# Kernel optimization log

Hardware: AMD Instinct MI355X
Metric: run time of the kernel (lower is better)

The kernel has to match this reference:

```python
import jax, jax.numpy as jnp
import numpy as np

MASK_SIZE = 28
IMG_H, IMG_W = 520, 704
NUM_GT = 128
NUM_PROP = 512


def box_iou(a, b):
    # a: [P,4], b: [G,4] in xyxy -> [P,G]
    area_a = (a[:, 2] - a[:, 0]) * (a[:, 3] - a[:, 1])
    area_b = (b[:, 2] - b[:, 0]) * (b[:, 3] - b[:, 1])
    lt = jnp.maximum(a[:, None, :2], b[None, :, :2])
    rb = jnp.minimum(a[:, None, 2:], b[None, :, 2:])
    wh = jnp.clip(rb - lt, 0.0)
    inter = wh[..., 0] * wh[..., 1]
    return inter / (area_a[:, None] + area_b[None, :] - inter)


def crop_resize_one(box, gidx, gt_masks):
    # Faithful to extract_mask_target: int-truncate box, clamp, crop, bilinear
    # resize (align_corners=False) to MASK_SIZE x MASK_SIZE.
    S = MASK_SIZE
    H, W = gt_masks.shape[1], gt_masks.shape[2]
    x1 = jnp.clip(box[0].astype(jnp.int32), 0, W - 1)
    y1 = jnp.clip(box[1].astype(jnp.int32), 0, H - 1)
    x2 = jnp.maximum(x1 + 1, jnp.minimum(box[2].astype(jnp.int32), W))
    y2 = jnp.maximum(y1 + 1, jnp.minimum(box[3].astype(jnp.int32), H))
    cwi = x2 - x1
    chi = y2 - y1
    cw = cwi.astype(jnp.float32)
    ch = chi.astype(jnp.float32)
    j = jnp.arange(S, dtype=jnp.float32)
    # source coords inside crop, border-clamped (PyTorch bilinear, align_corners=False)
    sx = jnp.clip((j + 0.5) * cw / S - 0.5, 0.0, cw - 1.0)
    sy = jnp.clip((j + 0.5) * ch / S - 0.5, 0.0, ch - 1.0)
    x0 = jnp.floor(sx)
    y0 = jnp.floor(sy)
    wx = sx - x0
    wy = sy - y0
    x0i = x0.astype(jnp.int32)
    y0i = y0.astype(jnp.int32)
    x1i = jnp.minimum(x0i + 1, cwi - 1)
    y1i = jnp.minimum(y0i + 1, chi - 1)
    m = gt_masks[gidx]  # [H, W]
    ax0 = x0i + x1
    ax1 = x1i + x1
    ay0 = y0i + y1
    ay1 = y1i + y1
    v00 = m[ay0[:, None], ax0[None, :]]
    v01 = m[ay0[:, None], ax1[None, :]]
    v10 = m[ay1[:, None], ax0[None, :]]
    v11 = m[ay1[:, None], ax1[None, :]]
    top = (1.0 - wx)[None, :] * v00 + wx[None, :] * v01
    bot = (1.0 - wx)[None, :] * v10 + wx[None, :] * v11
    return (1.0 - wy)[:, None] * top + wy[:, None] * bot  # [S, S]


def setup_inputs() -> dict:
    key = jax.random.key(0)
    k1, k2, k3, k4, k5 = jax.random.split(key, 5)
    # GT boxes: cell-like boxes inside a 520x704 image
    cx = jax.random.uniform(k1, (NUM_GT,), minval=50.0, maxval=IMG_W - 50.0)
    cy = jax.random.uniform(k2, (NUM_GT,), minval=50.0, maxval=IMG_H - 50.0)
    wh = jax.random.uniform(k3, (NUM_GT, 2), minval=20.0, maxval=80.0)
    gt_boxes = jnp.stack([cx - wh[:, 0] / 2, cy - wh[:, 1] / 2,
                          cx + wh[:, 0] / 2, cy + wh[:, 1] / 2], axis=1)
    # proposals: jittered copies of GT boxes -> realistic positive fraction
    reps = NUM_PROP // NUM_GT
    noise = jax.random.normal(k4, (NUM_PROP, 4)) * 4.0
    proposals = jnp.tile(gt_boxes, (reps, 1)) + noise
    # per-instance binary masks (float, as .float() in the torch code)
    gt_masks = (jax.random.uniform(k5, (NUM_GT, IMG_H, IMG_W)) < 0.3).astype(jnp.float32)
    mask_logits = jax.random.normal(jax.random.fold_in(key, 7),
                                    (NUM_PROP, 2, MASK_SIZE, MASK_SIZE), dtype=jnp.float32)
    return {"proposals": proposals, "gt_boxes": gt_boxes,
            "gt_masks": gt_masks, "mask_logits": mask_logits}


def reference(proposals, gt_boxes, gt_masks, mask_logits):
    S = MASK_SIZE
    ious = box_iou(proposals, gt_boxes)           # [P, G]
    max_ious = ious.max(axis=1)
    matched = jnp.argmax(ious, axis=1)            # [P]
    pos = (max_ious > 0.5).astype(jnp.float32)    # [P]
    matched_boxes = gt_boxes[matched]             # [P, 4]
    # batched crop + bilinear resize of matched GT masks (RoI-style gather)
    targets = jax.vmap(crop_resize_one, in_axes=(0, 0, None))(matched_boxes, matched, gt_masks)  # [P,S,S]
    logits = mask_logits[:, 1]                    # foreground channel [P,S,S]
    # stable BCE with logits
    bce = jnp.maximum(logits, 0.0) - logits * targets + jnp.log1p(jnp.exp(-jnp.abs(logits)))
    npos = pos.sum()
    loss_pos = jnp.sum(bce * pos[:, None, None]) / (jnp.maximum(npos, 1.0) * S * S)
    loss_neg = jnp.mean(mask_logits ** 2) * 0.01
    return jnp.where(npos > 0, loss_pos, loss_neg)
```

## Files before the change

kernel.cpp:

```cpp
#include <hip/hip_runtime.h>
#include <math.h>

#define NUM_GT   128
#define NUM_PROP 512
#define IMG_H    520
#define IMG_W    704
#define MS       28
#define LOGITS_N (NUM_PROP * 2 * MS * MS)

#define WS_MATCHED_OFF 256
#define WS_POS_OFF     (256 + NUM_PROP * 4)
#define WS_ZERO_BYTES  (256 + NUM_PROP * 8)

__global__ void match_kernel(const float* __restrict__ proposals,
                             const float* __restrict__ gt_boxes,
                             int* __restrict__ matched,
                             float* __restrict__ pos,
                             float* __restrict__ npos) {
    __shared__ float gb[NUM_GT * 4];
    for (int i = threadIdx.x; i < NUM_GT * 4; i += blockDim.x) gb[i] = gt_boxes[i];
    __syncthreads();

    int p = blockIdx.x * blockDim.x + threadIdx.x;
    if (p >= NUM_PROP) return;

    float ax1 = proposals[p * 4 + 0];
    float ay1 = proposals[p * 4 + 1];
    float ax2 = proposals[p * 4 + 2];
    float ay2 = proposals[p * 4 + 3];
    float area_a = (ax2 - ax1) * (ay2 - ay1);

    float best = -1e30f;
    int bi = 0;
    for (int g = 0; g < NUM_GT; ++g) {
        float bx1 = gb[g * 4 + 0];
        float by1 = gb[g * 4 + 1];
        float bx2 = gb[g * 4 + 2];
        float by2 = gb[g * 4 + 3];
        float area_b = (bx2 - bx1) * (by2 - by1);
        float ltx = fmaxf(ax1, bx1), lty = fmaxf(ay1, by1);
        float rbx = fminf(ax2, bx2), rby = fminf(ay2, by2);
        float w = fmaxf(rbx - ltx, 0.0f);
        float h = fmaxf(rby - lty, 0.0f);
        float inter = w * h;
        float iou = inter / (area_a + area_b - inter);
        if (iou > best) { best = iou; bi = g; }
    }
    matched[p] = bi;
    float ps = (best > 0.5f) ? 1.0f : 0.0f;
    pos[p] = ps;
    atomicAdd(npos, ps);
}

__global__ void bce_kernel(const float* __restrict__ gt_boxes,
                           const float* __restrict__ gt_masks,
                           const float* __restrict__ mask_logits,
                           const int* __restrict__ matched,
                           const float* __restrict__ pos,
                           float* __restrict__ bce_sum) {
    const int p = blockIdx.x;
    const int t = threadIdx.x;

    __shared__ int   s_gidx;
    __shared__ int   s_x0[MS], s_x1[MS], s_y0[MS], s_y1[MS];
    __shared__ float s_wx[MS], s_wy[MS];
    __shared__ float red[4];

    if (t == 0) s_gidx = matched[p];
    __syncthreads();
    const int g = s_gidx;

    const float b0 = gt_boxes[g * 4 + 0];
    const float b1 = gt_boxes[g * 4 + 1];
    const float b2 = gt_boxes[g * 4 + 2];
    const float b3 = gt_boxes[g * 4 + 3];

    int x1 = min(max((int)b0, 0), IMG_W - 1);
    int y1 = min(max((int)b1, 0), IMG_H - 1);
    int x2 = max(x1 + 1, min((int)b2, IMG_W));
    int y2 = max(y1 + 1, min((int)b3, IMG_H));
    int cwi = x2 - x1;
    int chi = y2 - y1;
    float cw = (float)cwi;
    float ch = (float)chi;

    if (t < MS) {
        float j = (float)t + 0.5f;
        float sx = fminf(fmaxf(j * cw / 28.0f - 0.5f, 0.0f), cw - 1.0f);
        float x0f = floorf(sx);
        int x0i = (int)x0f;
        s_wx[t] = sx - x0f;
        s_x0[t] = x0i + x1;
        s_x1[t] = min(x0i + 1, cwi - 1) + x1;

        float sy = fminf(fmaxf(j * ch / 28.0f - 0.5f, 0.0f), ch - 1.0f);
        float y0f = floorf(sy);
        int y0i = (int)y0f;
        s_wy[t] = sy - y0f;
        s_y0[t] = y0i + y1;
        s_y1[t] = min(y0i + 1, chi - 1) + y1;
    }
    __syncthreads();

    const float* m  = gt_masks + (size_t)g * IMG_H * IMG_W;
    const float* lg = mask_logits + ((size_t)p * 2 + 1) * (MS * MS);

    float acc = 0.0f;
    for (int idx = t; idx < MS * MS; idx += blockDim.x) {
        int i = idx / MS;
        int j = idx - i * MS;
        float wx = s_wx[j], wy = s_wy[i];
        const float* r0 = m + (size_t)s_y0[i] * IMG_W;
        const float* r1 = m + (size_t)s_y1[i] * IMG_W;
        int cx0 = s_x0[j], cx1 = s_x1[j];
        float v00 = r0[cx0], v01 = r0[cx1];
        float v10 = r1[cx0], v11 = r1[cx1];
        float top = (1.0f - wx) * v00 + wx * v01;
        float bot = (1.0f - wx) * v10 + wx * v11;
        float tv  = (1.0f - wy) * top + wy * bot;
        float l = lg[idx];
        float bce = fmaxf(l, 0.0f) - l * tv + log1pf(expf(-fabsf(l)));
        acc += bce;
    }

    float v = acc;
    #pragma unroll
    for (int o = 32; o > 0; o >>= 1) v += __shfl_down(v, o, 64);
    int lane = t & 63, wid = t >> 6;
    if (lane == 0) red[wid] = v;
    __syncthreads();
    if (t == 0) {
        float s = red[0] + red[1] + red[2] + red[3];
        atomicAdd(bce_sum, s * pos[p]);
    }
}

__global__ void sq_kernel(const float* __restrict__ mask_logits,
                          float* __restrict__ sqsum) {
    const int nvec = LOGITS_N / 4;
    const float4* src = (const float4*)mask_logits;
    float acc = 0.0f;
    for (int i = blockIdx.x * blockDim.x + threadIdx.x; i < nvec;
         i += gridDim.x * blockDim.x) {
        float4 x = src[i];
        acc += x.x * x.x + x.y * x.y + x.z * x.z + x.w * x.w;
    }
    float v = acc;
    #pragma unroll
    for (int o = 32; o > 0; o >>= 1) v += __shfl_down(v, o, 64);
    __shared__ float red[4];
    int lane = threadIdx.x & 63, wid = threadIdx.x >> 6;
    if (lane == 0) red[wid] = v;
    __syncthreads();
    if (threadIdx.x == 0) {
        float s = red[0] + red[1] + red[2] + red[3];
        atomicAdd(sqsum, s);
    }
}

__global__ void final_kernel(const float* __restrict__ acc, float* __restrict__ out) {
    float bce  = acc[0];
    float npos = acc[1];
    float sq   = acc[2];
    float loss_pos = bce / (fmaxf(npos, 1.0f) * (float)(MS * MS));
    float loss_neg = (sq / (float)LOGITS_N) * 0.01f;
    out[0] = (npos > 0.0f) ? loss_pos : loss_neg;
}

extern "C" void kernel_launch(void* const* d_in, const int* in_sizes, int n_in,
                              void* d_out, int out_size, void* d_ws, size_t ws_size,
                              hipStream_t stream) {
    const float* proposals   = (const float*)d_in[0];
    const float* gt_boxes    = (const float*)d_in[1];
    const float* gt_masks    = (const float*)d_in[2];
    const float* mask_logits = (const float*)d_in[3];
    float* out = (float*)d_out;

    float* acc     = (float*)d_ws;
    int*   matched = (int*)((char*)d_ws + WS_MATCHED_OFF);
    float* pos     = (float*)((char*)d_ws + WS_POS_OFF);

    hipMemsetAsync(d_ws, 0, WS_ZERO_BYTES, stream);

    match_kernel<<<(NUM_PROP + 255) / 256, 256, 0, stream>>>(proposals, gt_boxes,
                                                             matched, pos, acc + 1);
    bce_kernel<<<NUM_PROP, 256, 0, stream>>>(gt_boxes, gt_masks, mask_logits,
                                             matched, pos, acc + 0);
    sq_kernel<<<128, 256, 0, stream>>>(mask_logits, acc + 2);
    final_kernel<<<1, 1, 0, stream>>>(acc, out);
}
```

Measured before the change: 249.5 us.

## Fuse matching, BCE, square-sum and finalize into one kernel

Merges the IoU matching, crop-resize BCE, squared-logit sum and final loss computation into a single per-proposal kernel. Each block computes IoUs for its proposal in parallel across GT boxes with a shared-memory argmax reduction, and uses a last-block-done counter to write the final output. This removes three extra kernel launches, the intermediate matched/pos buffers and the serialized 128-iteration loop per thread. The cost is redundant loading of GT boxes in every block and an extra fence-and-atomic completion scheme.

```diff
diff --git a/kernel.cpp b/kernel.cpp
--- a/kernel.cpp
+++ b/kernel.cpp
@@ -8,83 +8,86 @@
 #define MS       28
 #define LOGITS_N (NUM_PROP * 2 * MS * MS)
 
-#define WS_MATCHED_OFF 256
-#define WS_POS_OFF     (256 + NUM_PROP * 4)
-#define WS_ZERO_BYTES  (256 + NUM_PROP * 8)
 
-__global__ void match_kernel(const float* __restrict__ proposals,
-                             const float* __restrict__ gt_boxes,
-                             int* __restrict__ matched,
-                             float* __restrict__ pos,
-                             float* __restrict__ npos) {
-    __shared__ float gb[NUM_GT * 4];
-    for (int i = threadIdx.x; i < NUM_GT * 4; i += blockDim.x) gb[i] = gt_boxes[i];
-    __syncthreads();
-
-    int p = blockIdx.x * blockDim.x + threadIdx.x;
-    if (p >= NUM_PROP) return;
-
-    float ax1 = proposals[p * 4 + 0];
-    float ay1 = proposals[p * 4 + 1];
-    float ax2 = proposals[p * 4 + 2];
-    float ay2 = proposals[p * 4 + 3];
-    float area_a = (ax2 - ax1) * (ay2 - ay1);
-
-    float best = -1e30f;
-    int bi = 0;
-    for (int g = 0; g < NUM_GT; ++g) {
-        float bx1 = gb[g * 4 + 0];
-        float by1 = gb[g * 4 + 1];
-        float bx2 = gb[g * 4 + 2];
-        float by2 = gb[g * 4 + 3];
-        float area_b = (bx2 - bx1) * (by2 - by1);
-        float ltx = fmaxf(ax1, bx1), lty = fmaxf(ay1, by1);
-        float rbx = fminf(ax2, bx2), rby = fminf(ay2, by2);
-        float w = fmaxf(rbx - ltx, 0.0f);
-        float h = fmaxf(rby - lty, 0.0f);
-        float inter = w * h;
-        float iou = inter / (area_a + area_b - inter);
-        if (iou > best) { best = iou; bi = g; }
-    }
-    matched[p] = bi;
-    float ps = (best > 0.5f) ? 1.0f : 0.0f;
-    pos[p] = ps;
-    atomicAdd(npos, ps);
-}
-
-__global__ void bce_kernel(const float* __restrict__ gt_boxes,
-                           const float* __restrict__ gt_masks,
-                           const float* __restrict__ mask_logits,
-                           const int* __restrict__ matched,
-                           const float* __restrict__ pos,
-                           float* __restrict__ bce_sum) {
+__global__ __launch_bounds__(256)
+void fused_kernel(const float* __restrict__ proposals,
+                  const float* __restrict__ gt_boxes,
+                  const float* __restrict__ gt_masks,
+                  const float* __restrict__ mask_logits,
+                  float* __restrict__ acc,
+                  float* __restrict__ out) {
     const int p = blockIdx.x;
     const int t = threadIdx.x;
 
-    __shared__ int   s_gidx;
+    __shared__ float s_gb[NUM_GT * 4];
+    __shared__ float s_iou[NUM_GT];
+    __shared__ int   s_idx[NUM_GT];
+    __shared__ int   s_g;
+    __shared__ float s_pos;
     __shared__ int   s_x0[MS], s_x1[MS], s_y0[MS], s_y1[MS];
     __shared__ float s_wx[MS], s_wy[MS];
-    __shared__ float red[4];
+    __shared__ float red_bce[4], red_sq[4];
 
-    if (t == 0) s_gidx = matched[p];
+    for (int i = t; i < NUM_GT * 4; i += 256) s_gb[i] = gt_boxes[i];
+
+    const float4* lp = (const float4*)(mask_logits + (size_t)p * 2 * MS * MS);
+    float sqacc = 0.0f;
+    for (int i = t; i < (2 * MS * MS) / 4; i += 256) {
+        float4 x = lp[i];
+        sqacc += x.x * x.x + x.y * x.y + x.z * x.z + x.w * x.w;
+    }
+
     __syncthreads();
-    const int g = s_gidx;
 
-    const float b0 = gt_boxes[g * 4 + 0];
-    const float b1 = gt_boxes[g * 4 + 1];
-    const float b2 = gt_boxes[g * 4 + 2];
-    const float b3 = gt_boxes[g * 4 + 3];
+    const float ax1 = proposals[p * 4 + 0];
+    const float ay1 = proposals[p * 4 + 1];
+    const float ax2 = proposals[p * 4 + 2];
+    const float ay2 = proposals[p * 4 + 3];
+    if (t < NUM_GT) {
+        float area_a = (ax2 - ax1) * (ay2 - ay1);
+        float bx1 = s_gb[t * 4 + 0];
+        float by1 = s_gb[t * 4 + 1];
+        float bx2 = s_gb[t * 4 + 2];
+        float by2 = s_gb[t * 4 + 3];
+        float area_b = (bx2 - bx1) * (by2 - by1);
+        float w = fmaxf(fminf(ax2, bx2) - fmaxf(ax1, bx1), 0.0f);
+        float h = fmaxf(fminf(ay2, by2) - fmaxf(ay1, by1), 0.0f);
+        float inter = w * h;
+        s_iou[t] = inter / (area_a + area_b - inter);
+        s_idx[t] = t;
+    }
+    __syncthreads();
 
-    int x1 = min(max((int)b0, 0), IMG_W - 1);
-    int y1 = min(max((int)b1, 0), IMG_H - 1);
-    int x2 = max(x1 + 1, min((int)b2, IMG_W));
-    int y2 = max(y1 + 1, min((int)b3, IMG_H));
-    int cwi = x2 - x1;
-    int chi = y2 - y1;
-    float cw = (float)cwi;
-    float ch = (float)chi;
+    for (int s = NUM_GT / 2; s > 0; s >>= 1) {
+        if (t < s) {
+            float a = s_iou[t], b = s_iou[t + s];
+            int ia = s_idx[t], ib = s_idx[t + s];
+            if (b > a || (b == a && ib < ia)) { s_iou[t] = b; s_idx[t] = ib; }
+        }
+        __syncthreads();
+    }
+    if (t == 0) {
+        s_g = s_idx[0];
+        s_pos = (s_iou[0] > 0.5f) ? 1.0f : 0.0f;
+    }
+    __syncthreads();
+
+    const int g = s_g;
 
     if (t < MS) {
+        float b0 = s_gb[g * 4 + 0];
+        float b1 = s_gb[g * 4 + 1];
+        float b2 = s_gb[g * 4 + 2];
+        float b3 = s_gb[g * 4 + 3];
+        int x1 = min(max((int)b0, 0), IMG_W - 1);
+        int y1 = min(max((int)b1, 0), IMG_H - 1);
+        int x2 = max(x1 + 1, min((int)b2, IMG_W));
+        int y2 = max(y1 + 1, min((int)b3, IMG_H));
+        int cwi = x2 - x1;
+        int chi = y2 - y1;
+        float cw = (float)cwi;
+        float ch = (float)chi;
+
         float j = (float)t + 0.5f;
         float sx = fminf(fmaxf(j * cw / 28.0f - 0.5f, 0.0f), cw - 1.0f);
         float x0f = floorf(sx);
@@ -105,8 +108,8 @@
     const float* m  = gt_masks + (size_t)g * IMG_H * IMG_W;
     const float* lg = mask_logits + ((size_t)p * 2 + 1) * (MS * MS);
 
-    float acc = 0.0f;
-    for (int idx = t; idx < MS * MS; idx += blockDim.x) {
+    float bceacc = 0.0f;
+    for (int idx = t; idx < MS * MS; idx += 256) {
         int i = idx / MS;
         int j = idx - i * MS;
         float wx = s_wx[j], wy = s_wy[i];
@@ -119,52 +122,36 @@
         float bot = (1.0f - wx) * v10 + wx * v11;
         float tv  = (1.0f - wy) * top + wy * bot;
         float l = lg[idx];
-        float bce = fmaxf(l, 0.0f) - l * tv + log1pf(expf(-fabsf(l)));
-        acc += bce;
+        bceacc += fmaxf(l, 0.0f) - l * tv + log1pf(expf(-fabsf(l)));
     }
 
-    float v = acc;
+    float vb = bceacc, vs = sqacc;
     #pragma unroll
-    for (int o = 32; o > 0; o >>= 1) v += __shfl_down(v, o, 64);
+    for (int o = 32; o > 0; o >>= 1) {
+        vb += __shfl_down(vb, o, 64);
+        vs += __shfl_down(vs, o, 64);
+    }
     int lane = t & 63, wid = t >> 6;
-    if (lane == 0) red[wid] = v;
+    if (lane == 0) { red_bce[wid] = vb; red_sq[wid] = vs; }
     __syncthreads();
+
     if (t == 0) {
-        float s = red[0] + red[1] + red[2] + red[3];
-        atomicAdd(bce_sum, s * pos[p]);
+        float bce_s = red_bce[0] + red_bce[1] + red_bce[2] + red_bce[3];
+        float sq_s  = red_sq[0] + red_sq[1] + red_sq[2] + red_sq[3];
+        atomicAdd(acc + 0, bce_s * s_pos);
+        atomicAdd(acc + 1, s_pos);
+        atomicAdd(acc + 2, sq_s);
+        __threadfence();
+        unsigned done = atomicAdd((unsigned*)(acc + 3), 1u);
+        if (done == NUM_PROP - 1) {
+            float bce  = atomicAdd(acc + 0, 0.0f);
+            float npos = atomicAdd(acc + 1, 0.0f);
+            float sq   = atomicAdd(acc + 2, 0.0f);
+            float loss_pos = bce / (fmaxf(npos, 1.0f) * (float)(MS * MS));
+            float loss_neg = (sq / (float)LOGITS_N) * 0.01f;
+            out[0] = (npos > 0.0f) ? loss_pos : loss_neg;
+        }
     }
-}
-
-__global__ void sq_kernel(const float* __restrict__ mask_logits,
-                          float* __restrict__ sqsum) {
-    const int nvec = LOGITS_N / 4;
-    const float4* src = (const float4*)mask_logits;
-    float acc = 0.0f;
-    for (int i = blockIdx.x * blockDim.x + threadIdx.x; i < nvec;
-         i += gridDim.x * blockDim.x) {
-        float4 x = src[i];
-        acc += x.x * x.x + x.y * x.y + x.z * x.z + x.w * x.w;
-    }
-    float v = acc;
-    #pragma unroll
-    for (int o = 32; o > 0; o >>= 1) v += __shfl_down(v, o, 64);
-    __shared__ float red[4];
-    int lane = threadIdx.x & 63, wid = threadIdx.x >> 6;
-    if (lane == 0) red[wid] = v;
-    __syncthreads();
-    if (threadIdx.x == 0) {
-        float s = red[0] + red[1] + red[2] + red[3];
-        atomicAdd(sqsum, s);
-    }
-}
-
-__global__ void final_kernel(const float* __restrict__ acc, float* __restrict__ out) {
-    float bce  = acc[0];
-    float npos = acc[1];
-    float sq   = acc[2];
-    float loss_pos = bce / (fmaxf(npos, 1.0f) * (float)(MS * MS));
-    float loss_neg = (sq / (float)LOGITS_N) * 0.01f;
-    out[0] = (npos > 0.0f) ? loss_pos : loss_neg;
 }
 
 extern "C" void kernel_launch(void* const* d_in, const int* in_sizes, int n_in,
@@ -175,17 +162,9 @@
     const float* gt_masks    = (const float*)d_in[2];
     const float* mask_logits = (const float*)d_in[3];
     float* out = (float*)d_out;
+    float* acc = (float*)d_ws;
 
-    float* acc     = (float*)d_ws;
-    int*   matched = (int*)((char*)d_ws + WS_MATCHED_OFF);
-    float* pos     = (float*)((char*)d_ws + WS_POS_OFF);
-
-    hipMemsetAsync(d_ws, 0, WS_ZERO_BYTES, stream);
-
-    match_kernel<<<(NUM_PROP + 255) / 256, 256, 0, stream>>>(proposals, gt_boxes,
-                                                             matched, pos, acc + 1);
-    bce_kernel<<<NUM_PROP, 256, 0, stream>>>(gt_boxes, gt_masks, mask_logits,
-                                             matched, pos, acc + 0);
-    sq_kernel<<<128, 256, 0, stream>>>(mask_logits, acc + 2);
-    final_kernel<<<1, 1, 0, stream>>>(acc, out);
+    hipMemsetAsync(d_ws, 0, 16, stream);
+    fused_kernel<<<NUM_PROP, 256, 0, stream>>>(proposals, gt_boxes, gt_masks,
+                                               mask_logits, acc, out);
 }
```

Measured after the change: 253.0 us. No clear change (+1.4%).
